# Performance work log

Measured on AMD Instinct MI355X. Metric: run time of the kernel, lower is better.

Reference implementation:

```python
import jax, jax.numpy as jnp
import numpy as np
import math

NUM_CLASSES = 15
IN_CH = 256
FEAT_CH = 256
STRIDES = (8, 16, 32, 64, 128)
SCALES = (4.0,)
RATIOS = (6.0,)
ANGLES = (-0.125 * math.pi, 0.125 * math.pi, 0.375 * math.pi, 0.625 * math.pi)
NUM_ANCHORS = len(SCALES) * len(RATIOS) * len(ANGLES)  # 4
WH_RATIO_CLIP = 1e-6


def conv2d(x, w, b, pad):
    y = jax.lax.conv_general_dilated(
        x, w, window_strides=(1, 1), padding=[(pad, pad), (pad, pad)],
        dimension_numbers=("NCHW", "OIHW", "NCHW"))
    return y + b[None, :, None, None]


def gen_grid_anchors(base_size, feat_h, feat_w, stride):
    # AnchorGeneratorRotated (S2ANet style): base anchors [A,5] = (xc,yc,w,h,angle)
    scales = jnp.asarray(SCALES, jnp.float32)
    ratios = jnp.asarray(RATIOS, jnp.float32)
    angles = jnp.asarray(ANGLES, jnp.float32)
    h_ratios = jnp.sqrt(ratios)
    w_ratios = 1.0 / h_ratios
    ones = jnp.ones_like(angles)
    ws = (base_size * w_ratios[:, None, None] * scales[None, :, None] * ones[None, None, :]).reshape(-1)
    hs = (base_size * h_ratios[:, None, None] * scales[None, :, None] * ones[None, None, :]).reshape(-1)
    ang = jnp.tile(angles, ratios.size * scales.size)
    ctr = 0.5 * (base_size - 1.0)
    base = jnp.stack([jnp.full_like(ws, ctr), jnp.full_like(ws, ctr), ws, hs, ang], axis=-1)  # [A,5]
    xx = jnp.arange(feat_w, dtype=jnp.float32) * stride
    yy = jnp.arange(feat_h, dtype=jnp.float32) * stride
    gx, gy = jnp.meshgrid(xx, yy)  # [H,W]
    zeros = jnp.zeros_like(gx)
    shift = jnp.stack([gx, gy, zeros, zeros, zeros], axis=-1)  # [H,W,5]
    return base[None, None] + shift[:, :, None, :]  # [H,W,A,5]


def norm_angle(a):
    # normalize to [-pi/4, 3pi/4)
    return (a + 0.25 * jnp.pi) % jnp.pi - 0.25 * jnp.pi


def rboxes_decode(anchors, deltas):
    # is_encode_relative=False branch of delta2rbox
    max_ratio = abs(math.log(WH_RATIO_CLIP))
    dx, dy, dw, dh, da = jnp.split(deltas, 5, axis=-1)
    rx, ry, rw, rh, ra = jnp.split(anchors, 5, axis=-1)
    dw = jnp.clip(dw, -max_ratio, max_ratio)
    dh = jnp.clip(dh, -max_ratio, max_ratio)
    gx = dx * rw + rx
    gy = dy * rh + ry
    gw = rw * jnp.exp(dw)
    gh = rh * jnp.exp(dh)
    ga = norm_angle(da + ra)
    return jnp.concatenate([gx, gy, gw, gh, ga], axis=-1)


def _head_level(x, stride, p):
    B, _, H, W = x.shape
    # reg tower (2 stacked 3x3 conv + relu)
    r = jax.nn.relu(conv2d(x, p["reg_w0"], p["reg_b0"], 1))
    r = jax.nn.relu(conv2d(r, p["reg_w1"], p["reg_b1"], 1))
    bbox = conv2d(r, p["reg_head_w"], p["reg_head_b"], 0)
    bbox = bbox.transpose(0, 2, 3, 1).reshape(B, H, W, NUM_ANCHORS, 5)
    conf = conv2d(r, p["conf_w"], p["conf_b"], 0)
    conf = conf.transpose(0, 2, 3, 1).reshape(B, H, W, NUM_ANCHORS, 1)
    anchors = gen_grid_anchors(float(stride), H, W, float(stride))  # [H,W,A,5]
    dec = rboxes_decode(anchors[None], jax.lax.stop_gradient(bbox))  # [B,H,W,A,5]
    # refine-anchor selection: pick decoded box of max-confidence anchor per location
    conf_sig = jax.nn.sigmoid(jax.lax.stop_gradient(conf))[..., 0]  # [B,H,W,A]
    idx = jnp.argmax(conf_sig, axis=3)  # [B,H,W]
    refine = jnp.take_along_axis(dec, idx[..., None, None], axis=3)[:, :, :, 0, :]  # [B,H,W,5]
    # cls tower
    c = jax.nn.relu(conv2d(x, p["cls_w0"], p["cls_b0"], 1))
    c = jax.nn.relu(conv2d(c, p["cls_w1"], p["cls_b1"], 1))
    cls = conv2d(c, p["cls_head_w"], p["cls_head_b"], 0)
    cls = cls.transpose(0, 2, 3, 1).reshape(B, H, W, NUM_ANCHORS, NUM_CLASSES)
    # per-image scores as in get_bboxes: sigmoid(cls) * sigmoid(conf)
    scores = jax.nn.sigmoid(cls.reshape(B, -1, NUM_CLASSES)) * jax.nn.sigmoid(conf.reshape(B, -1, 1))
    return scores, dec.reshape(B, -1, 5), refine


def setup_inputs() -> dict:
    key = jax.random.key(0)
    ks = jax.random.split(key, 24)
    B = 8
    sizes = [(128, 128), (64, 64), (32, 32), (16, 16), (8, 8)]
    inp = {}
    for i, (h, w) in enumerate(sizes):
        inp[f"feat{i}"] = jax.random.normal(ks[i], (B, IN_CH, h, w), jnp.float32)
    std = 0.01
    bias_cls = float(-np.log((1 - 0.01) / 0.01))
    inp["reg_w0"] = jax.random.normal(ks[5], (FEAT_CH, IN_CH, 3, 3), jnp.float32) * std
    inp["reg_b0"] = jnp.zeros((FEAT_CH,), jnp.float32)
    inp["reg_w1"] = jax.random.normal(ks[6], (FEAT_CH, FEAT_CH, 3, 3), jnp.float32) * std
    inp["reg_b1"] = jnp.zeros((FEAT_CH,), jnp.float32)
    inp["cls_w0"] = jax.random.normal(ks[7], (FEAT_CH, IN_CH, 3, 3), jnp.float32) * std
    inp["cls_b0"] = jnp.zeros((FEAT_CH,), jnp.float32)
    inp["cls_w1"] = jax.random.normal(ks[8], (FEAT_CH, FEAT_CH, 3, 3), jnp.float32) * std
    inp["cls_b1"] = jnp.zeros((FEAT_CH,), jnp.float32)
    inp["reg_head_w"] = jax.random.normal(ks[9], (5 * NUM_ANCHORS, FEAT_CH, 1, 1), jnp.float32) * std
    inp["reg_head_b"] = jnp.zeros((5 * NUM_ANCHORS,), jnp.float32)
    inp["cls_head_w"] = jax.random.normal(ks[10], (NUM_CLASSES * NUM_ANCHORS, FEAT_CH, 1, 1), jnp.float32) * std
    inp["cls_head_b"] = jnp.full((NUM_CLASSES * NUM_ANCHORS,), bias_cls, jnp.float32)
    inp["conf_w"] = jax.random.normal(ks[11], (NUM_ANCHORS, FEAT_CH, 1, 1), jnp.float32) * std
    inp["conf_b"] = jnp.full((NUM_ANCHORS,), bias_cls, jnp.float32)
    return inp


def reference(feat0, feat1, feat2, feat3, feat4,
              reg_w0, reg_b0, reg_w1, reg_b1,
              cls_w0, cls_b0, cls_w1, cls_b1,
              reg_head_w, reg_head_b, cls_head_w, cls_head_b,
              conf_w, conf_b):
    p = dict(reg_w0=reg_w0, reg_b0=reg_b0, reg_w1=reg_w1, reg_b1=reg_b1,
             cls_w0=cls_w0, cls_b0=cls_b0, cls_w1=cls_w1, cls_b1=cls_b1,
             reg_head_w=reg_head_w, reg_head_b=reg_head_b,
             cls_head_w=cls_head_w, cls_head_b=cls_head_b,
             conf_w=conf_w, conf_b=conf_b)
    feats = [feat0, feat1, feat2, feat3, feat4]
    scores_ls, boxes_ls = [], []
    for x, s in zip(feats, STRIDES):
        sc, bx, _ = _head_level(x, s, p)
        scores_ls.append(sc)
        boxes_ls.append(bx)
    scores = jnp.concatenate(scores_ls, axis=1)  # [B, N_total, num_classes]
    boxes = jnp.concatenate(boxes_ls, axis=1)    # [B, N_total, 5]
    return scores, boxes
```

## Files before the change

kernel.cpp:

```cpp
#include <hip/hip_runtime.h>


typedef __attribute__((ext_vector_type(8))) _Float16 f16x8;
typedef __attribute__((ext_vector_type(4))) float f32x4;

#define SCORES_TOTAL 10475520ull

__device__ __forceinline__ unsigned short f2h(float f) {
  union { _Float16 h; unsigned short u; } x;
  x.h = (_Float16)f;
  return x.u;
}

__device__ __forceinline__ float sigmf(float x) {
  return 1.0f / (1.0f + expf(-x));
}

__device__ __forceinline__ void gload_lds16(const unsigned short* g,
                                            unsigned short* l) {
  __builtin_amdgcn_global_load_lds(
      (const __attribute__((address_space(1))) unsigned int*)g,
      (__attribute__((address_space(3))) unsigned int*)l, 16, 0, 0);
}

__device__ __forceinline__ unsigned lds_addr(const void* p) {
  return (unsigned)(size_t)(const __attribute__((address_space(3))) char*)p;
}

#define DSR(d, va, off) \
  asm volatile("ds_read_b128 %0, %1 offset:" off : "=v"(d) : "v"(va))

__device__ __forceinline__ void lvl_lookup(int gm, int& logW, int& mbase) {
  if (gm < 131072) { logW = 7; mbase = 0; }
  else if (gm < 163840) { logW = 6; mbase = 131072; }
  else if (gm < 172032) { logW = 5; mbase = 163840; }
  else if (gm < 174080) { logW = 4; mbase = 172032; }
  else { logW = 3; mbase = 174080; }
}

__global__ __launch_bounds__(256) void prep_convw(
    const float* __restrict__ w0, const float* __restrict__ w1,
    const float* __restrict__ w2, const float* __restrict__ w3,
    unsigned short* __restrict__ wtout) {
  int g = blockIdx.x * 256 + threadIdx.x;
  int q = g >> 16;
  int wsel = q / 9;
  int kk = q - wsel * 9;
  int r = g & 65535;
  int oc = r >> 8, ic = r & 255;
  const float* src = (wsel == 0) ? w0 : (wsel == 1) ? w1 : (wsel == 2) ? w2 : w3;
  float v = src[(size_t)(oc * 256 + ic) * 9 + kk];
  wtout[(size_t)wsel * 589824 + (size_t)((kk << 8) + oc) * 256 + ic] = f2h(v);
}

__global__ __launch_bounds__(256) void prep_small(
    const float* __restrict__ clsh, const float* __restrict__ regh,
    const float* __restrict__ confw,
    unsigned short* __restrict__ wc, unsigned short* __restrict__ wh,
    unsigned short* __restrict__ zp) {
  int g = blockIdx.x * 256 + threadIdx.x;
  if (g < 16384) {
    int row = g >> 8, ic = g & 255;
    float v = (row < 60) ? clsh[row * 256 + ic] : 0.0f;
    wc[g] = f2h(v);
  } else if (g < 24576) {
    int gg = g - 16384;
    int row = gg >> 8, ic = gg & 255;
    float v = 0.0f;
    if (row < 20) v = regh[row * 256 + ic];
    else if (row < 24) v = confw[(row - 20) * 256 + ic];
    wh[gg] = f2h(v);
  } else if (g < 24640) {
    zp[g - 24576] = 0;
  }
}

__global__ __launch_bounds__(256) void to_nhwc_all(
    const float* __restrict__ f0, const float* __restrict__ f1,
    const float* __restrict__ f2, const float* __restrict__ f3,
    const float* __restrict__ f4, unsigned short* __restrict__ out) {
  __shared__ unsigned short L[64][258];
  const int t = threadIdx.x;
  const int gm0 = blockIdx.x * 64;
  int logW, mbase;
  const float* in;
  if (gm0 < 131072) { logW = 7; mbase = 0; in = f0; }
  else if (gm0 < 163840) { logW = 6; mbase = 131072; in = f1; }
  else if (gm0 < 172032) { logW = 5; mbase = 163840; in = f2; }
  else if (gm0 < 174080) { logW = 4; mbase = 172032; in = f3; }
  else { logW = 3; mbase = 174080; in = f4; }
  const int logHW = 2 * logW;
  const int HW = 1 << logHW;
  const int lm0 = gm0 - mbase;
  const int b = lm0 >> logHW;
  const int hw0 = lm0 & (HW - 1);
#pragma unroll
  for (int it = 0; it < 16; ++it) {
    int c = it * 16 + (t >> 4);
    int j4 = (t & 15) * 4;
    float4 v = *reinterpret_cast<const float4*>(
        in + (size_t)(b * 256 + c) * HW + hw0 + j4);
    L[j4 + 0][c] = f2h(v.x);
    L[j4 + 1][c] = f2h(v.y);
    L[j4 + 2][c] = f2h(v.z);
    L[j4 + 3][c] = f2h(v.w);
  }
  __syncthreads();
#pragma unroll
  for (int it = 0; it < 16; ++it) {
    int j = it * 4 + (t >> 6);
    int c4 = (t & 63) * 4;
    unsigned v0 = (unsigned)L[j][c4 + 0] | ((unsigned)L[j][c4 + 1] << 16);
    unsigned v1 = (unsigned)L[j][c4 + 2] | ((unsigned)L[j][c4 + 3] << 16);
    uint2 v = make_uint2(v0, v1);
    *reinterpret_cast<uint2*>(out + ((size_t)(gm0 + j) << 8) + c4) = v;
  }
}

__global__ __launch_bounds__(512, 2) void conv256(
    const unsigned short* __restrict__ xin,
    const unsigned short* __restrict__ wt,
    const float* __restrict__ bias,
    const unsigned short* __restrict__ zp,
    unsigned short* __restrict__ yout,
    int gm_base) {
  __shared__ unsigned short pool[65536];
  const int t = threadIdx.x;
  const int lane = t & 63;
  const int wv = t >> 6;
  const int wm = wv >> 2;
  const int wn = wv & 3;
  const int gm0 = gm_base + blockIdx.x * 256;
  int logW, mbase;
  lvl_lookup(gm0, logW, mbase);
  const int logHW = 2 * logW;
  const int H = 1 << logW, W = H;
  const int HWm1 = (1 << logHW) - 1, Wm1 = W - 1;

  const int schk = ((lane & 7) ^ ((lane >> 3) & 7)) << 3;
  int hj[4], wj[4];
  const unsigned short* aptr[4];
  const unsigned short* bptr[4];
#pragma unroll
  for (int i = 0; i < 4; ++i) {
    int r = (wv << 5) + (i << 3) + (lane >> 3);
    int gm = gm0 + r;
    int lm = gm - mbase;
    int hw = lm & HWm1;
    hj[i] = hw >> logW;
    wj[i] = hw & Wm1;
    aptr[i] = xin + ((size_t)gm << 8) + schk;
    bptr[i] = wt + ((size_t)r << 8) + schk;
  }

  f32x4 acc[8][4];
#pragma unroll
  for (int i = 0; i < 8; ++i)
#pragma unroll
    for (int j = 0; j < 4; ++j) acc[i][j] = (f32x4){0.f, 0.f, 0.f, 0.f};

  const int l15 = lane & 15;
  const int arow0 = (wm << 7) + l15;
  const int brow0 = (wn << 6) + l15;
  int achkb[2];
#pragma unroll
  for (int ks = 0; ks < 2; ++ks)
    achkb[ks] = ((((ks << 2) + (lane >> 4)) ^ (lane & 7)) << 4);

  const unsigned pbase = lds_addr(pool);
  unsigned ava0 = pbase + (arow0 << 7) + achkb[0];
  unsigned ava1 = pbase + (arow0 << 7) + achkb[1];
  unsigned bva0 = pbase + 65536 + (brow0 << 7) + achkb[0];
  unsigned bva1 = pbase + 65536 + (brow0 << 7) + achkb[1];

  auto STAGE_A = [&](int p, int bsel) {
    int icq = p / 9;
    int kk = p - icq * 9;
    int k3 = kk / 3;
    int dy = k3 - 1, dxv = kk - k3 * 3 - 1;
    int moff = ((dy << logW) + dxv) << 8;
    int ico = icq << 6;
    unsigned short* dst = pool + (bsel << 14) + (wv << 11);
#pragma unroll
    for (int i = 0; i < 4; ++i) {
      bool valid = ((unsigned)(hj[i] + dy) < (unsigned)H) &
                   ((unsigned)(wj[i] + dxv) < (unsigned)W);
      const unsigned short* g = valid ? (aptr[i] + moff + ico) : zp;
      gload_lds16(g, dst + (i << 9));
    }
  };
  auto STAGE_B = [&](int p, int bsel) {
    int icq = p / 9;
    int kk = p - icq * 9;
    int boff = (kk << 16) + (icq << 6);
    unsigned short* dst = pool + 32768 + (bsel << 14) + (wv << 11);
#pragma unroll
    for (int i = 0; i < 4; ++i)
      gload_lds16(bptr[i] + boff, dst + (i << 9));
  };

  STAGE_A(0, 0);
  STAGE_B(0, 0);
  asm volatile("s_waitcnt vmcnt(0)");
  __builtin_amdgcn_s_barrier();

#pragma unroll 1
  for (int tt = 0; tt < 36; ++tt) {
    const int nb = (tt & 1) ^ 1;
    f16x8 a0, a1, a2, a3, b00, b01, b02, b03, b10, b11, b12, b13;

    DSR(a0, ava0, "0");
    DSR(a1, ava0, "2048");
    DSR(a2, ava0, "4096");
    DSR(a3, ava0, "6144");
    DSR(b00, bva0, "0");
    DSR(b01, bva0, "2048");
    DSR(b02, bva0, "4096");
    DSR(b03, bva0, "6144");
    if (tt < 35) STAGE_A(tt + 1, nb);
    __builtin_amdgcn_s_barrier();
    asm volatile("s_waitcnt lgkmcnt(0)");
    __builtin_amdgcn_sched_barrier(0);
    __builtin_amdgcn_s_setprio(1);
    acc[0][0] = __builtin_amdgcn_mfma_f32_16x16x32_f16(a0, b00, acc[0][0], 0, 0, 0);
    acc[0][1] = __builtin_amdgcn_mfma_f32_16x16x32_f16(a0, b01, acc[0][1], 0, 0, 0);
    acc[0][2] = __builtin_amdgcn_mfma_f32_16x16x32_f16(a0, b02, acc[0][2], 0, 0, 0);
    acc[0][3] = __builtin_amdgcn_mfma_f32_16x16x32_f16(a0, b03, acc[0][3], 0, 0, 0);
    acc[1][0] = __builtin_amdgcn_mfma_f32_16x16x32_f16(a1, b00, acc[1][0], 0, 0, 0);
    acc[1][1] = __builtin_amdgcn_mfma_f32_16x16x32_f16(a1, b01, acc[1][1], 0, 0, 0);
    acc[1][2] = __builtin_amdgcn_mfma_f32_16x16x32_f16(a1, b02, acc[1][2], 0, 0, 0);
    acc[1][3] = __builtin_amdgcn_mfma_f32_16x16x32_f16(a1, b03, acc[1][3], 0, 0, 0);
    acc[2][0] = __builtin_amdgcn_mfma_f32_16x16x32_f16(a2, b00, acc[2][0], 0, 0, 0);
    acc[2][1] = __builtin_amdgcn_mfma_f32_16x16x32_f16(a2, b01, acc[2][1], 0, 0, 0);
    acc[2][2] = __builtin_amdgcn_mfma_f32_16x16x32_f16(a2, b02, acc[2][2], 0, 0, 0);
    acc[2][3] = __builtin_amdgcn_mfma_f32_16x16x32_f16(a2, b03, acc[2][3], 0, 0, 0);
    acc[3][0] = __builtin_amdgcn_mfma_f32_16x16x32_f16(a3, b00, acc[3][0], 0, 0, 0);
    acc[3][1] = __builtin_amdgcn_mfma_f32_16x16x32_f16(a3, b01, acc[3][1], 0, 0, 0);
    acc[3][2] = __builtin_amdgcn_mfma_f32_16x16x32_f16(a3, b02, acc[3][2], 0, 0, 0);
    acc[3][3] = __builtin_amdgcn_mfma_f32_16x16x32_f16(a3, b03, acc[3][3], 0, 0, 0);
    __builtin_amdgcn_s_setprio(0);
    __builtin_amdgcn_s_barrier();

    DSR(a0, ava0, "8192");
    DSR(a1, ava0, "10240");
    DSR(a2, ava0, "12288");
    DSR(a3, ava0, "14336");
    if (tt < 35) STAGE_B(tt + 1, nb);
    __builtin_amdgcn_s_barrier();
    asm volatile("s_waitcnt lgkmcnt(0)");
    __builtin_amdgcn_sched_barrier(0);
    __builtin_amdgcn_s_setprio(1);
    acc[4][0] = __builtin_amdgcn_mfma_f32_16x16x32_f16(a0, b00, acc[4][0], 0, 0, 0);
    acc[4][1] = __builtin_amdgcn_mfma_f32_16x16x32_f16(a0, b01, acc[4][1], 0, 0, 0);
    acc[4][2] = __builtin_amdgcn_mfma_f32_16x16x32_f16(a0, b02, acc[4][2], 0, 0, 0);
    acc[4][3] = __builtin_amdgcn_mfma_f32_16x16x32_f16(a0, b03, acc[4][3], 0, 0, 0);
    acc[5][0] = __builtin_amdgcn_mfma_f32_16x16x32_f16(a1, b00, acc[5][0], 0, 0, 0);
    acc[5][1] = __builtin_amdgcn_mfma_f32_16x16x32_f16(a1, b01, acc[5][1], 0, 0, 0);
    acc[5][2] = __builtin_amdgcn_mfma_f32_16x16x32_f16(a1, b02, acc[5][2], 0, 0, 0);
    acc[5][3] = __builtin_amdgcn_mfma_f32_16x16x32_f16(a1, b03, acc[5][3], 0, 0, 0);
    acc[6][0] = __builtin_amdgcn_mfma_f32_16x16x32_f16(a2, b00, acc[6][0], 0, 0, 0);
    acc[6][1] = __builtin_amdgcn_mfma_f32_16x16x32_f16(a2, b01, acc[6][1], 0, 0, 0);
    acc[6][2] = __builtin_amdgcn_mfma_f32_16x16x32_f16(a2, b02, acc[6][2], 0, 0, 0);
    acc[6][3] = __builtin_amdgcn_mfma_f32_16x16x32_f16(a2, b03, acc[6][3], 0, 0, 0);
    acc[7][0] = __builtin_amdgcn_mfma_f32_16x16x32_f16(a3, b00, acc[7][0], 0, 0, 0);
    acc[7][1] = __builtin_amdgcn_mfma_f32_16x16x32_f16(a3, b01, acc[7][1], 0, 0, 0);
    acc[7][2] = __builtin_amdgcn_mfma_f32_16x16x32_f16(a3, b02, acc[7][2], 0, 0, 0);
    acc[7][3] = __builtin_amdgcn_mfma_f32_16x16x32_f16(a3, b03, acc[7][3], 0, 0, 0);
    __builtin_amdgcn_s_setprio(0);
    __builtin_amdgcn_s_barrier();

    DSR(a0, ava1, "0");
    DSR(a1, ava1, "2048");
    DSR(a2, ava1, "4096");
    DSR(a3, ava1, "6144");
    DSR(b10, bva1, "0");
    DSR(b11, bva1, "2048");
    DSR(b12, bva1, "4096");
    DSR(b13, bva1, "6144");
    __builtin_amdgcn_s_barrier();
    asm volatile("s_waitcnt lgkmcnt(0)");
    __builtin_amdgcn_sched_barrier(0);
    __builtin_amdgcn_s_setprio(1);
    acc[0][0] = __builtin_amdgcn_mfma_f32_16x16x32_f16(a0, b10, acc[0][0], 0, 0, 0);
    acc[0][1] = __builtin_amdgcn_mfma_f32_16x16x32_f16(a0, b11, acc[0][1], 0, 0, 0);
    acc[0][2] = __builtin_amdgcn_mfma_f32_16x16x32_f16(a0, b12, acc[0][2], 0, 0, 0);
    acc[0][3] = __builtin_amdgcn_mfma_f32_16x16x32_f16(a0, b13, acc[0][3], 0, 0, 0);
    acc[1][0] = __builtin_amdgcn_mfma_f32_16x16x32_f16(a1, b10, acc[1][0], 0, 0, 0);
    acc[1][1] = __builtin_amdgcn_mfma_f32_16x16x32_f16(a1, b11, acc[1][1], 0, 0, 0);
    acc[1][2] = __builtin_amdgcn_mfma_f32_16x16x32_f16(a1, b12, acc[1][2], 0, 0, 0);
    acc[1][3] = __builtin_amdgcn_mfma_f32_16x16x32_f16(a1, b13, acc[1][3], 0, 0, 0);
    acc[2][0] = __builtin_amdgcn_mfma_f32_16x16x32_f16(a2, b10, acc[2][0], 0, 0, 0);
    acc[2][1] = __builtin_amdgcn_mfma_f32_16x16x32_f16(a2, b11, acc[2][1], 0, 0, 0);
    acc[2][2] = __builtin_amdgcn_mfma_f32_16x16x32_f16(a2, b12, acc[2][2], 0, 0, 0);
    acc[2][3] = __builtin_amdgcn_mfma_f32_16x16x32_f16(a2, b13, acc[2][3], 0, 0, 0);
    acc[3][0] = __builtin_amdgcn_mfma_f32_16x16x32_f16(a3, b10, acc[3][0], 0, 0, 0);
    acc[3][1] = __builtin_amdgcn_mfma_f32_16x16x32_f16(a3, b11, acc[3][1], 0, 0, 0);
    acc[3][2] = __builtin_amdgcn_mfma_f32_16x16x32_f16(a3, b12, acc[3][2], 0, 0, 0);
    acc[3][3] = __builtin_amdgcn_mfma_f32_16x16x32_f16(a3, b13, acc[3][3], 0, 0, 0);
    __builtin_amdgcn_s_setprio(0);
    __builtin_amdgcn_s_barrier();

    DSR(a0, ava1, "8192");
    DSR(a1, ava1, "10240");
    DSR(a2, ava1, "12288");
    DSR(a3, ava1, "14336");
    asm volatile("s_waitcnt vmcnt(0)");
    __builtin_amdgcn_s_barrier();
    asm volatile("s_waitcnt lgkmcnt(0)");
    __builtin_amdgcn_sched_barrier(0);
    __builtin_amdgcn_s_setprio(1);
    acc[4][0] = __builtin_amdgcn_mfma_f32_16x16x32_f16(a0, b10, acc[4][0], 0, 0, 0);
    acc[4][1] = __builtin_amdgcn_mfma_f32_16x16x32_f16(a0, b11, acc[4][1], 0, 0, 0);
    acc[4][2] = __builtin_amdgcn_mfma_f32_16x16x32_f16(a0, b12, acc[4][2], 0, 0, 0);
    acc[4][3] = __builtin_amdgcn_mfma_f32_16x16x32_f16(a0, b13, acc[4][3], 0, 0, 0);
    acc[5][0] = __builtin_amdgcn_mfma_f32_16x16x32_f16(a1, b10, acc[5][0], 0, 0, 0);
    acc[5][1] = __builtin_amdgcn_mfma_f32_16x16x32_f16(a1, b11, acc[5][1], 0, 0, 0);
    acc[5][2] = __builtin_amdgcn_mfma_f32_16x16x32_f16(a1, b12, acc[5][2], 0, 0, 0);
    acc[5][3] = __builtin_amdgcn_mfma_f32_16x16x32_f16(a1, b13, acc[5][3], 0, 0, 0);
    acc[6][0] = __builtin_amdgcn_mfma_f32_16x16x32_f16(a2, b10, acc[6][0], 0, 0, 0);
    acc[6][1] = __builtin_amdgcn_mfma_f32_16x16x32_f16(a2, b11, acc[6][1], 0, 0, 0);
    acc[6][2] = __builtin_amdgcn_mfma_f32_16x16x32_f16(a2, b12, acc[6][2], 0, 0, 0);
    acc[6][3] = __builtin_amdgcn_mfma_f32_16x16x32_f16(a2, b13, acc[6][3], 0, 0, 0);
    acc[7][0] = __builtin_amdgcn_mfma_f32_16x16x32_f16(a3, b10, acc[7][0], 0, 0, 0);
    acc[7][1] = __builtin_amdgcn_mfma_f32_16x16x32_f16(a3, b11, acc[7][1], 0, 0, 0);
    acc[7][2] = __builtin_amdgcn_mfma_f32_16x16x32_f16(a3, b12, acc[7][2], 0, 0, 0);
    acc[7][3] = __builtin_amdgcn_mfma_f32_16x16x32_f16(a3, b13, acc[7][3], 0, 0, 0);
    __builtin_amdgcn_s_setprio(0);
    __builtin_amdgcn_s_barrier();

    ava0 ^= 32768u;
    ava1 ^= 32768u;
    bva0 ^= 32768u;
    bva1 ^= 32768u;
  }
  __syncthreads();

  {
    const int eg = (lane >> 4) << 2;
    const int el = lane & 15;
#pragma unroll
    for (int nf = 0; nf < 4; ++nf) {
      float bi = bias[(wn << 6) + (nf << 4) + el];
#pragma unroll
      for (int mf = 0; mf < 8; ++mf)
#pragma unroll
        for (int r = 0; r < 4; ++r) {
          int wrow = (wm << 7) + (mf << 4) + eg + r;
          pool[(wrow << 8) + (wn << 6) + (nf << 4) + el] =
              f2h(fmaxf(acc[mf][nf][r] + bi, 0.0f));
        }
    }
  }
  __syncthreads();
  {
    const int row = t >> 1;
    const int half = t & 1;
    const unsigned short* src = pool + (row << 8) + (half << 7);
    unsigned short* dst = yout + ((size_t)(gm0 + row) << 8) + (half << 7);
#pragma unroll
    for (int q = 0; q < 16; ++q)
      reinterpret_cast<uint4*>(dst)[q] =
          reinterpret_cast<const uint4*>(src)[q];
  }
}

__global__ __launch_bounds__(256) void head24_mfma(
    const unsigned short* __restrict__ t2,
    const unsigned short* __restrict__ wh,
    const float* __restrict__ regb, const float* __restrict__ confb,
    float* __restrict__ hbuf) {
  const int t = threadIdx.x, lane = t & 63, wv = t >> 6;
  const int rowb = blockIdx.x * 256 + wv * 64;
  const int kgrp = (lane >> 4) << 3;
  const int l15 = lane & 15;
  f32x4 acc[4][2];
#pragma unroll
  for (int i = 0; i < 4; ++i)
#pragma unroll
    for (int j = 0; j < 2; ++j) acc[i][j] = (f32x4){0.f, 0.f, 0.f, 0.f};
#pragma unroll
  for (int k0 = 0; k0 < 256; k0 += 32) {
    f16x8 a[4], b[2];
#pragma unroll
    for (int mf = 0; mf < 4; ++mf)
      a[mf] = *reinterpret_cast<const f16x8*>(
          t2 + (((size_t)(rowb + (mf << 4) + l15)) << 8) + k0 + kgrp);
#pragma unroll
    for (int nf = 0; nf < 2; ++nf)
      b[nf] = *reinterpret_cast<const f16x8*>(
          wh + (size_t)(((nf << 4) + l15) << 8) + k0 + kgrp);
#pragma unroll
    for (int mf = 0; mf < 4; ++mf)
#pragma unroll
      for (int nf = 0; nf < 2; ++nf)
        acc[mf][nf] = __builtin_amdgcn_mfma_f32_16x16x32_f16(
            a[mf], b[nf], acc[mf][nf], 0, 0, 0);
  }
#pragma unroll
  for (int nf = 0; nf < 2; ++nf) {
    int c = (nf << 4) + l15;
    if (c < 24) {
      float bi = (c < 20) ? regb[c] : confb[c - 20];
#pragma unroll
      for (int mf = 0; mf < 4; ++mf)
#pragma unroll
        for (int r = 0; r < 4; ++r) {
          int m = rowb + (mf << 4) + ((lane >> 4) << 2) + r;
          hbuf[(size_t)m * 24 + c] = acc[mf][nf][r] + bi;
        }
    }
  }
}

__global__ __launch_bounds__(256) void cls_scores(
    const unsigned short* __restrict__ t2,
    const unsigned short* __restrict__ wcw,
    const float* __restrict__ clsb,
    const float* __restrict__ hbuf,
    float* __restrict__ outs, int gm_base) {
  const int t = threadIdx.x, lane = t & 63, wv = t >> 6;
  const int gm0 = gm_base + blockIdx.x * 256;
  int logW, mbase, lvl_off;
  if (gm0 < 131072) { logW = 7; mbase = 0; lvl_off = 0; }
  else if (gm0 < 163840) { logW = 6; mbase = 131072; lvl_off = 65536; }
  else if (gm0 < 172032) { logW = 5; mbase = 163840; lvl_off = 81920; }
  else if (gm0 < 174080) { logW = 4; mbase = 172032; lvl_off = 86016; }
  else { logW = 3; mbase = 174080; lvl_off = 87040; }
  const int logHW = 2 * logW, HWm1 = (1 << logHW) - 1;
  const int rowb = gm0 + wv * 64;
  const int kgrp = (lane >> 4) << 3;
  const int l15 = lane & 15;
  f32x4 acc[4][4];
#pragma unroll
  for (int i = 0; i < 4; ++i)
#pragma unroll
    for (int j = 0; j < 4; ++j) acc[i][j] = (f32x4){0.f, 0.f, 0.f, 0.f};
#pragma unroll
  for (int k0 = 0; k0 < 256; k0 += 32) {
    f16x8 a[4], b[4];
#pragma unroll
    for (int mf = 0; mf < 4; ++mf)
      a[mf] = *reinterpret_cast<const f16x8*>(
          t2 + (((size_t)(rowb + (mf << 4) + l15)) << 8) + k0 + kgrp);
#pragma unroll
    for (int nf = 0; nf < 4; ++nf)
      b[nf] = *reinterpret_cast<const f16x8*>(
          wcw + (size_t)(((nf << 4) + l15) << 8) + k0 + kgrp);
#pragma unroll
    for (int mf = 0; mf < 4; ++mf)
#pragma unroll
      for (int nf = 0; nf < 4; ++nf)
        acc[mf][nf] = __builtin_amdgcn_mfma_f32_16x16x32_f16(
            a[mf], b[nf], acc[mf][nf], 0, 0, 0);
  }
#pragma unroll
  for (int nf = 0; nf < 4; ++nf) {
    int c = (nf << 4) + l15;
    if (c < 60) {
      int ai = c / 15, ci = c - ai * 15;
      float bi = clsb[c];
#pragma unroll
      for (int mf = 0; mf < 4; ++mf)
#pragma unroll
        for (int r = 0; r < 4; ++r) {
          int m = rowb + (mf << 4) + ((lane >> 4) << 2) + r;
          float logit = acc[mf][nf][r] + bi;
          float conf = hbuf[(size_t)m * 24 + 20 + ai];
          float sc = sigmf(logit) * sigmf(conf);
          int lm = m - mbase;
          int b = lm >> logHW;
          int hw = lm & HWm1;
          int loc = lvl_off + (hw << 2) + ai;
          outs[(size_t)b * 1309440 + (size_t)loc * 15 + ci] = sc;
        }
    }
  }
}

__global__ __launch_bounds__(256) void decode_all(
    const float* __restrict__ hbuf, float* __restrict__ outb) {
  int tid = blockIdx.x * 256 + threadIdx.x;
  if (tid >= 174592 * 4) return;
  int m = tid >> 2, a = tid & 3;
  int logW, mbase, lvl_off;
  float stride;
  if (m < 131072) { logW = 7; mbase = 0; lvl_off = 0; stride = 8.f; }
  else if (m < 163840) { logW = 6; mbase = 131072; lvl_off = 65536; stride = 16.f; }
  else if (m < 172032) { logW = 5; mbase = 163840; lvl_off = 81920; stride = 32.f; }
  else if (m < 174080) { logW = 4; mbase = 172032; lvl_off = 86016; stride = 64.f; }
  else { logW = 3; mbase = 174080; lvl_off = 87040; stride = 128.f; }
  const int logHW = 2 * logW;
  const float ANG[4] = {-0.39269908169872414f, 0.39269908169872414f,
                        1.1780972450961724f, 1.9634954084936207f};
  const float* d = hbuf + (size_t)m * 24 + a * 5;
  float dx = d[0], dy = d[1], dw = d[2], dh = d[3], da = d[4];
  int lm = m - mbase;
  int b = lm >> logHW, hw = lm & ((1 << logHW) - 1);
  int h = hw >> logW, w = hw & ((1 << logW) - 1);
  float ctr = 0.5f * (stride - 1.0f);
  float rx = w * stride + ctr, ry = h * stride + ctr;
  float rw = stride * 1.6329931618554521f;
  float rh = stride * 9.7979589711327124f;
  const float MR = 13.815510557964274f;
  dw = fminf(fmaxf(dw, -MR), MR);
  dh = fminf(fmaxf(dh, -MR), MR);
  float gx = dx * rw + rx;
  float gy = dy * rh + ry;
  float gw = rw * expf(dw);
  float gh = rh * expf(dh);
  float v = da + ANG[a] + 0.7853981633974483f;
  float r = fmodf(v, 3.14159265358979323846f);
  if (r < 0.0f) r += 3.14159265358979323846f;
  float ga = r - 0.7853981633974483f;
  int loc = lvl_off + (hw << 2) + a;
  size_t base = (size_t)b * 436480 + (size_t)loc * 5;
  outb[base + 0] = gx;
  outb[base + 1] = gy;
  outb[base + 2] = gw;
  outb[base + 3] = gh;
  outb[base + 4] = ga;
}

extern "C" void kernel_launch(void* const* d_in, const int* in_sizes, int n_in,
                              void* d_out, int out_size, void* d_ws,
                              size_t ws_size, hipStream_t stream) {
  const float* feats[5];
  for (int i = 0; i < 5; ++i) feats[i] = (const float*)d_in[i];
  const float* reg_w0 = (const float*)d_in[5];
  const float* reg_b0 = (const float*)d_in[6];
  const float* reg_w1 = (const float*)d_in[7];
  const float* reg_b1 = (const float*)d_in[8];
  const float* cls_w0 = (const float*)d_in[9];
  const float* cls_b0 = (const float*)d_in[10];
  const float* cls_w1 = (const float*)d_in[11];
  const float* cls_b1 = (const float*)d_in[12];
  const float* reg_head_w = (const float*)d_in[13];
  const float* reg_head_b = (const float*)d_in[14];
  const float* cls_head_w = (const float*)d_in[15];
  const float* cls_head_b = (const float*)d_in[16];
  const float* conf_w = (const float*)d_in[17];
  const float* conf_b = (const float*)d_in[18];

  unsigned short* ws = (unsigned short*)d_ws;
  unsigned short* t1r = ws + 44695552ull;
  unsigned short* t1c = ws + 78249984ull;
  unsigned short* wt4 = ws + 111804416ull;
  unsigned short* wh = ws + 114163712ull;
  unsigned short* wc = ws + 114171904ull;
  unsigned short* zp = ws + 114188288ull;
  float* hbuf_all = (float*)((char*)d_ws + 228376704ull);

  prep_convw<<<9216, 256, 0, stream>>>(reg_w0, reg_w1, cls_w0, cls_w1, wt4);
  prep_small<<<97, 256, 0, stream>>>(cls_head_w, reg_head_w, conf_w, wc, wh,
                                     zp);
  to_nhwc_all<<<2728, 256, 0, stream>>>(feats[0], feats[1], feats[2], feats[3],
                                        feats[4], ws);

  float* scores = (float*)d_out;
  float* boxes = (float*)d_out + SCORES_TOTAL;

  static const int gbase[2] = {0, 131072};
  static const int gM[2] = {131072, 43520};
  for (int g = 0; g < 2; ++g) {
    const int base = gbase[g];
    const int M = gM[g];
    const int nb = M / 256;
    const size_t bofs = ((size_t)base << 8);
    unsigned short* t1r_v = t1r - bofs;
    unsigned short* t1c_v = t1c - bofs;
    conv256<<<nb, 512, 0, stream>>>(ws, wt4 + 0ull * 589824, reg_b0, zp, t1r_v,
                                    base);
    conv256<<<nb, 512, 0, stream>>>(ws, wt4 + 2ull * 589824, cls_b0, zp, t1c_v,
                                    base);
    conv256<<<nb, 512, 0, stream>>>(t1r_v, wt4 + 1ull * 589824, reg_b1, zp, ws,
                                    base);
    head24_mfma<<<nb, 256, 0, stream>>>(ws + bofs, wh, reg_head_b, conf_b,
                                        hbuf_all + (size_t)base * 24);
    conv256<<<nb, 512, 0, stream>>>(t1c_v, wt4 + 3ull * 589824, cls_b1, zp, ws,
                                    base);
    cls_scores<<<nb, 256, 0, stream>>>(ws, wc, cls_head_b, hbuf_all, scores,
                                       base);
  }
  decode_all<<<(174592 * 4 + 255) / 256, 256, 0, stream>>>(hbuf_all, boxes);
}
```

Baseline: 1.076 ms.

## Double A-fragment registers and drop intra-iteration barriers in conv GEMM loop

The main MFMA loop now holds eight A fragments, so LDS reads for the next sub-block are issued before the current MFMAs run. Partial lgkmcnt waits replace full drains, and all but one s_barrier per iteration are removed, leaving a single vmcnt(0) and barrier at the end. This aims to overlap LDS reads with MFMA work and cut synchronisation stalls. It raises VGPR pressure, and it relies on LDS double buffering alone to avoid races now that STAGE_A and STAGE_B writes are no longer fenced by mid-iteration barriers.

```diff
diff --git a/kernel.cpp b/kernel.cpp
--- a/kernel.cpp
+++ b/kernel.cpp
@@ -207,7 +207,8 @@
 #pragma unroll 1
   for (int tt = 0; tt < 36; ++tt) {
     const int nb = (tt & 1) ^ 1;
-    f16x8 a0, a1, a2, a3, b00, b01, b02, b03, b10, b11, b12, b13;
+    f16x8 a0, a1, a2, a3, a4, a5, a6, a7;
+    f16x8 b00, b01, b02, b03, b10, b11, b12, b13;
 
     DSR(a0, ava0, "0");
     DSR(a1, ava0, "2048");
@@ -217,9 +218,13 @@
     DSR(b01, bva0, "2048");
     DSR(b02, bva0, "4096");
     DSR(b03, bva0, "6144");
+    DSR(a4, ava0, "8192");
+    DSR(a5, ava0, "10240");
+    DSR(a6, ava0, "12288");
+    DSR(a7, ava0, "14336");
     if (tt < 35) STAGE_A(tt + 1, nb);
-    __builtin_amdgcn_s_barrier();
-    asm volatile("s_waitcnt lgkmcnt(0)");
+
+    asm volatile("s_waitcnt lgkmcnt(4)");
     __builtin_amdgcn_sched_barrier(0);
     __builtin_amdgcn_s_setprio(1);
     acc[0][0] = __builtin_amdgcn_mfma_f32_16x16x32_f16(a0, b00, acc[0][0], 0, 0, 0);
@@ -239,35 +244,6 @@
     acc[3][2] = __builtin_amdgcn_mfma_f32_16x16x32_f16(a3, b02, acc[3][2], 0, 0, 0);
     acc[3][3] = __builtin_amdgcn_mfma_f32_16x16x32_f16(a3, b03, acc[3][3], 0, 0, 0);
     __builtin_amdgcn_s_setprio(0);
-    __builtin_amdgcn_s_barrier();
-
-    DSR(a0, ava0, "8192");
-    DSR(a1, ava0, "10240");
-    DSR(a2, ava0, "12288");
-    DSR(a3, ava0, "14336");
-    if (tt < 35) STAGE_B(tt + 1, nb);
-    __builtin_amdgcn_s_barrier();
-    asm volatile("s_waitcnt lgkmcnt(0)");
-    __builtin_amdgcn_sched_barrier(0);
-    __builtin_amdgcn_s_setprio(1);
-    acc[4][0] = __builtin_amdgcn_mfma_f32_16x16x32_f16(a0, b00, acc[4][0], 0, 0, 0);
-    acc[4][1] = __builtin_amdgcn_mfma_f32_16x16x32_f16(a0, b01, acc[4][1], 0, 0, 0);
-    acc[4][2] = __builtin_amdgcn_mfma_f32_16x16x32_f16(a0, b02, acc[4][2], 0, 0, 0);
-    acc[4][3] = __builtin_amdgcn_mfma_f32_16x16x32_f16(a0, b03, acc[4][3], 0, 0, 0);
-    acc[5][0] = __builtin_amdgcn_mfma_f32_16x16x32_f16(a1, b00, acc[5][0], 0, 0, 0);
-    acc[5][1] = __builtin_amdgcn_mfma_f32_16x16x32_f16(a1, b01, acc[5][1], 0, 0, 0);
-    acc[5][2] = __builtin_amdgcn_mfma_f32_16x16x32_f16(a1, b02, acc[5][2], 0, 0, 0);
-    acc[5][3] = __builtin_amdgcn_mfma_f32_16x16x32_f16(a1, b03, acc[5][3], 0, 0, 0);
-    acc[6][0] = __builtin_amdgcn_mfma_f32_16x16x32_f16(a2, b00, acc[6][0], 0, 0, 0);
-    acc[6][1] = __builtin_amdgcn_mfma_f32_16x16x32_f16(a2, b01, acc[6][1], 0, 0, 0);
-    acc[6][2] = __builtin_amdgcn_mfma_f32_16x16x32_f16(a2, b02, acc[6][2], 0, 0, 0);
-    acc[6][3] = __builtin_amdgcn_mfma_f32_16x16x32_f16(a2, b03, acc[6][3], 0, 0, 0);
-    acc[7][0] = __builtin_amdgcn_mfma_f32_16x16x32_f16(a3, b00, acc[7][0], 0, 0, 0);
-    acc[7][1] = __builtin_amdgcn_mfma_f32_16x16x32_f16(a3, b01, acc[7][1], 0, 0, 0);
-    acc[7][2] = __builtin_amdgcn_mfma_f32_16x16x32_f16(a3, b02, acc[7][2], 0, 0, 0);
-    acc[7][3] = __builtin_amdgcn_mfma_f32_16x16x32_f16(a3, b03, acc[7][3], 0, 0, 0);
-    __builtin_amdgcn_s_setprio(0);
-    __builtin_amdgcn_s_barrier();
 
     DSR(a0, ava1, "0");
     DSR(a1, ava1, "2048");
@@ -277,8 +253,35 @@
     DSR(b11, bva1, "2048");
     DSR(b12, bva1, "4096");
     DSR(b13, bva1, "6144");
-    __builtin_amdgcn_s_barrier();
-    asm volatile("s_waitcnt lgkmcnt(0)");
+    if (tt < 35) STAGE_B(tt + 1, nb);
+
+    asm volatile("s_waitcnt lgkmcnt(8)");
+    __builtin_amdgcn_sched_barrier(0);
+    __builtin_amdgcn_s_setprio(1);
+    acc[4][0] = __builtin_amdgcn_mfma_f32_16x16x32_f16(a4, b00, acc[4][0], 0, 0, 0);
+    acc[4][1] = __builtin_amdgcn_mfma_f32_16x16x32_f16(a4, b01, acc[4][1], 0, 0, 0);
+    acc[4][2] = __builtin_amdgcn_mfma_f32_16x16x32_f16(a4, b02, acc[4][2], 0, 0, 0);
+    acc[4][3] = __builtin_amdgcn_mfma_f32_16x16x32_f16(a4, b03, acc[4][3], 0, 0, 0);
+    acc[5][0] = __builtin_amdgcn_mfma_f32_16x16x32_f16(a5, b00, acc[5][0], 0, 0, 0);
+    acc[5][1] = __builtin_amdgcn_mfma_f32_16x16x32_f16(a5, b01, acc[5][1], 0, 0, 0);
+    acc[5][2] = __builtin_amdgcn_mfma_f32_16x16x32_f16(a5, b02, acc[5][2], 0, 0, 0);
+    acc[5][3] = __builtin_amdgcn_mfma_f32_16x16x32_f16(a5, b03, acc[5][3], 0, 0, 0);
+    acc[6][0] = __builtin_amdgcn_mfma_f32_16x16x32_f16(a6, b00, acc[6][0], 0, 0, 0);
+    acc[6][1] = __builtin_amdgcn_mfma_f32_16x16x32_f16(a6, b01, acc[6][1], 0, 0, 0);
+    acc[6][2] = __builtin_amdgcn_mfma_f32_16x16x32_f16(a6, b02, acc[6][2], 0, 0, 0);
+    acc[6][3] = __builtin_amdgcn_mfma_f32_16x16x32_f16(a6, b03, acc[6][3], 0, 0, 0);
+    acc[7][0] = __builtin_amdgcn_mfma_f32_16x16x32_f16(a7, b00, acc[7][0], 0, 0, 0);
+    acc[7][1] = __builtin_amdgcn_mfma_f32_16x16x32_f16(a7, b01, acc[7][1], 0, 0, 0);
+    acc[7][2] = __builtin_amdgcn_mfma_f32_16x16x32_f16(a7, b02, acc[7][2], 0, 0, 0);
+    acc[7][3] = __builtin_amdgcn_mfma_f32_16x16x32_f16(a7, b03, acc[7][3], 0, 0, 0);
+    __builtin_amdgcn_s_setprio(0);
+
+    DSR(a4, ava1, "8192");
+    DSR(a5, ava1, "10240");
+    DSR(a6, ava1, "12288");
+    DSR(a7, ava1, "14336");
+
+    asm volatile("s_waitcnt lgkmcnt(4)");
     __builtin_amdgcn_sched_barrier(0);
     __builtin_amdgcn_s_setprio(1);
     acc[0][0] = __builtin_amdgcn_mfma_f32_16x16x32_f16(a0, b10, acc[0][0], 0, 0, 0);
@@ -298,36 +301,30 @@
     acc[3][2] = __builtin_amdgcn_mfma_f32_16x16x32_f16(a3, b12, acc[3][2], 0, 0, 0);
     acc[3][3] = __builtin_amdgcn_mfma_f32_16x16x32_f16(a3, b13, acc[3][3], 0, 0, 0);
     __builtin_amdgcn_s_setprio(0);
-    __builtin_amdgcn_s_barrier();
-
-    DSR(a0, ava1, "8192");
-    DSR(a1, ava1, "10240");
-    DSR(a2, ava1, "12288");
-    DSR(a3, ava1, "14336");
-    asm volatile("s_waitcnt vmcnt(0)");
-    __builtin_amdgcn_s_barrier();
+
     asm volatile("s_waitcnt lgkmcnt(0)");
     __builtin_amdgcn_sched_barrier(0);
     __builtin_amdgcn_s_setprio(1);
-    acc[4][0] = __builtin_amdgcn_mfma_f32_16x16x32_f16(a0, b10, acc[4][0], 0, 0, 0);
-    acc[4][1] = __builtin_amdgcn_mfma_f32_16x16x32_f16(a0, b11, acc[4][1], 0, 0, 0);
-    acc[4][2] = __builtin_amdgcn_mfma_f32_16x16x32_f16(a0, b12, acc[4][2], 0, 0, 0);
-    acc[4][3] = __builtin_amdgcn_mfma_f32_16x16x32_f16(a0, b13, acc[4][3], 0, 0, 0);
-    acc[5][0] = __builtin_amdgcn_mfma_f32_16x16x32_f16(a1, b10, acc[5][0], 0, 0, 0);
-    acc[5][1] = __builtin_amdgcn_mfma_f32_16x16x32_f16(a1, b11, acc[5][1], 0, 0, 0);
-    acc[5][2] = __builtin_amdgcn_mfma_f32_16x16x32_f16(a1, b12, acc[5][2], 0, 0, 0);
-    acc[5][3] = __builtin_amdgcn_mfma_f32_16x16x32_f16(a1, b13, acc[5][3], 0, 0, 0);
-    acc[6][0] = __builtin_amdgcn_mfma_f32_16x16x32_f16(a2, b10, acc[6][0], 0, 0, 0);
-    acc[6][1] = __builtin_amdgcn_mfma_f32_16x16x32_f16(a2, b11, acc[6][1], 0, 0, 0);
-    acc[6][2] = __builtin_amdgcn_mfma_f32_16x16x32_f16(a2, b12, acc[6][2], 0, 0, 0);
-    acc[6][3] = __builtin_amdgcn_mfma_f32_16x16x32_f16(a2, b13, acc[6][3], 0, 0, 0);
-    acc[7][0] = __builtin_amdgcn_mfma_f32_16x16x32_f16(a3, b10, acc[7][0], 0, 0, 0);
-    acc[7][1] = __builtin_amdgcn_mfma_f32_16x16x32_f16(a3, b11, acc[7][1], 0, 0, 0);
-    acc[7][2] = __builtin_amdgcn_mfma_f32_16x16x32_f16(a3, b12, acc[7][2], 0, 0, 0);
-    acc[7][3] = __builtin_amdgcn_mfma_f32_16x16x32_f16(a3, b13, acc[7][3], 0, 0, 0);
+    acc[4][0] = __builtin_amdgcn_mfma_f32_16x16x32_f16(a4, b10, acc[4][0], 0, 0, 0);
+    acc[4][1] = __builtin_amdgcn_mfma_f32_16x16x32_f16(a4, b11, acc[4][1], 0, 0, 0);
+    acc[4][2] = __builtin_amdgcn_mfma_f32_16x16x32_f16(a4, b12, acc[4][2], 0, 0, 0);
+    acc[4][3] = __builtin_amdgcn_mfma_f32_16x16x32_f16(a4, b13, acc[4][3], 0, 0, 0);
+    acc[5][0] = __builtin_amdgcn_mfma_f32_16x16x32_f16(a5, b10, acc[5][0], 0, 0, 0);
+    acc[5][1] = __builtin_amdgcn_mfma_f32_16x16x32_f16(a5, b11, acc[5][1], 0, 0, 0);
+    acc[5][2] = __builtin_amdgcn_mfma_f32_16x16x32_f16(a5, b12, acc[5][2], 0, 0, 0);
+    acc[5][3] = __builtin_amdgcn_mfma_f32_16x16x32_f16(a5, b13, acc[5][3], 0, 0, 0);
+    acc[6][0] = __builtin_amdgcn_mfma_f32_16x16x32_f16(a6, b10, acc[6][0], 0, 0, 0);
+    acc[6][1] = __builtin_amdgcn_mfma_f32_16x16x32_f16(a6, b11, acc[6][1], 0, 0, 0);
+    acc[6][2] = __builtin_amdgcn_mfma_f32_16x16x32_f16(a6, b12, acc[6][2], 0, 0, 0);
+    acc[6][3] = __builtin_amdgcn_mfma_f32_16x16x32_f16(a6, b13, acc[6][3], 0, 0, 0);
+    acc[7][0] = __builtin_amdgcn_mfma_f32_16x16x32_f16(a7, b10, acc[7][0], 0, 0, 0);
+    acc[7][1] = __builtin_amdgcn_mfma_f32_16x16x32_f16(a7, b11, acc[7][1], 0, 0, 0);
+    acc[7][2] = __builtin_amdgcn_mfma_f32_16x16x32_f16(a7, b12, acc[7][2], 0, 0, 0);
+    acc[7][3] = __builtin_amdgcn_mfma_f32_16x16x32_f16(a7, b13, acc[7][3], 0, 0, 0);
     __builtin_amdgcn_s_setprio(0);
+
+    asm volatile("s_waitcnt vmcnt(0)");
     __builtin_amdgcn_s_barrier();
-
     ava0 ^= 32768u;
     ava1 ^= 32768u;
     bva0 ^= 32768u;
```

New measurement: 994.9 us. 7.5% less time.
